# Performance work log

Measured on AMD Instinct MI355X. Metric: run time of the kernel, lower is better.

## Reference

```python
import math
import jax, jax.numpy as jnp
import numpy as np

B, T, M, S, D, H = 16, 512, 8, 32, 256, 4
HD = D // H


def setup_inputs() -> dict:
    key = jax.random.key(0)
    ks = jax.random.split(key, 16)
    w = 1.0 / math.sqrt(D)
    return {
        'q_temporal': jax.random.normal(ks[0], (B, T, M, D), jnp.float32),
        'q_static': jax.random.normal(ks[1], (B, S, D), jnp.float32),
        'k_temporal': jax.random.normal(ks[2], (B, T, M, D), jnp.float32),
        'v_temporal': jax.random.normal(ks[3], (B, T, M, D), jnp.float32),
        'k_static': jax.random.normal(ks[4], (B, S, D), jnp.float32),
        'v_static': jax.random.normal(ks[5], (B, S, D), jnp.float32),
        'q_w': jax.random.normal(ks[6], (D, D), jnp.float32) * w,
        'q_b': jax.random.normal(ks[7], (D,), jnp.float32) * w,
        'k_w': jax.random.normal(ks[8], (D, D), jnp.float32) * w,
        'k_b': jax.random.normal(ks[9], (D,), jnp.float32) * w,
        'v_w': jax.random.normal(ks[10], (D, D), jnp.float32) * w,
        'v_b': jax.random.normal(ks[11], (D,), jnp.float32) * w,
        'o_w': jax.random.normal(ks[12], (D, D), jnp.float32) * w,
        'o_b': jax.random.normal(ks[13], (D,), jnp.float32) * w,
        'mask_temporal': jax.random.randint(ks[14], (B, T, M), 0, 2).astype(jnp.int32),
        'mask_fcst': jax.random.randint(ks[15], (B, T, M), 0, 2).astype(jnp.int32),
        'mask_static': jnp.ones((B, S), jnp.int32),
    }


def _lin(x, w, b):
    # torch.nn.Linear: y = x @ W^T + b
    return x @ w.T + b


def reference(q_temporal, q_static, k_temporal, v_temporal, k_static, v_static,
              q_w, q_b, k_w, k_b, v_w, v_b, o_w, o_b,
              mask_temporal, mask_fcst, mask_static):
    scale = 1.0 / math.sqrt(HD)

    def heads5(x):  # [B,T,M,D] -> [B,H,T,M,HD]
        return x.reshape(B, T, M, H, HD).transpose(0, 3, 1, 2, 4)

    def heads3(x):  # [B,S,D] -> [B,H,S,HD]
        return x.reshape(B, -1, H, HD).transpose(0, 2, 1, 3)

    Qt = heads5(_lin(q_temporal, q_w, q_b))
    Kt = heads5(_lin(k_temporal, k_w, k_b))
    Vt = heads5(_lin(v_temporal, v_w, v_b))
    Qs = heads3(_lin(q_static, q_w, q_b))
    Ks = heads3(_lin(k_static, k_w, k_b))
    Vs = heads3(_lin(v_static, v_w, v_b))

    # additive masks: 0 where valid (==1), -inf where padded
    mt = jnp.where(mask_temporal == 1, 0.0, -jnp.inf).astype(Qt.dtype)  # [B,T,M]
    ms = jnp.where(mask_static == 1, 0.0, -jnp.inf).astype(Qt.dtype)    # [B,S]

    # ---- temporal query branch ----
    # temp_temp: per-timestep modality-vs-modality attention, column key mask
    Qt_Kt = jnp.einsum('bhtmd,bhtnd->bhtmn', Qt, Kt) * scale + mt[:, None, :, None, :]
    # temp_static: temporal queries vs static keys
    Qt_Ks = jnp.einsum('bhtmd,bhsd->bhtms', Qt, Ks) * scale + ms[:, None, None, None, :]
    tw = jax.nn.softmax(jnp.concatenate([Qt_Kt, Qt_Ks], axis=-1), axis=-1)  # [B,H,T,M,M+S]
    QKV_t = (jnp.einsum('bhtmn,bhtnd->bhtmd', tw[..., :M], Vt)
             + jnp.einsum('bhtms,bhsd->bhtmd', tw[..., M:], Vs))
    out_t = _lin(QKV_t.transpose(0, 2, 3, 1, 4).reshape(B, T, M, D), o_w, o_b)

    # ---- static query branch ----
    Ktf = Kt.reshape(B, H, T * M, HD)  # flatten (T,M) key axis
    Vtf = Vt.reshape(B, H, T * M, HD)
    Qs_Kt = jnp.einsum('bhqd,bhkd->bhqk', Qs, Ktf) * scale + mt.reshape(B, 1, 1, T * M)
    Qs_Ks = jnp.einsum('bhqd,bhsd->bhqs', Qs, Ks) * scale + ms[:, None, None, :]
    sw = jax.nn.softmax(jnp.concatenate([Qs_Kt, Qs_Ks], axis=-1), axis=-1)  # [B,H,S,T*M+S]
    QKV_s = (jnp.einsum('bhqk,bhkd->bhqd', sw[..., :T * M], Vtf)
             + jnp.einsum('bhqs,bhsd->bhqd', sw[..., T * M:], Vs))
    out_s = _lin(QKV_s.transpose(0, 2, 1, 3).reshape(B, S, D), o_w, o_b)

    return (out_t, out_s, tw, sw)
```

## Files before the change

kernel.cpp:

```cpp
#include <hip/hip_runtime.h>

#define B_   16
#define T_   512
#define M_   8
#define S_   32
#define D_   256
#define H_   4
#define HD_  64
#define TM_  4096
#define NKT  40
#define NKS  4128

typedef unsigned short u16;
typedef __attribute__((ext_vector_type(8))) short bf16x8;
typedef __attribute__((ext_vector_type(4))) float f32x4;

__device__ __forceinline__ u16 f2b(float f) {
    union { float f; unsigned u; } v; v.f = f;
    unsigned r = v.u + 0x7FFF + ((v.u >> 16) & 1);
    return (u16)(r >> 16);
}
__device__ __forceinline__ float blo(unsigned u) {
    union { unsigned i; float f; } v; v.i = u << 16; return v.f;
}
__device__ __forceinline__ float bhi(unsigned u) {
    union { unsigned i; float f; } v; v.i = u & 0xFFFF0000u; return v.f;
}
__device__ __forceinline__ float b2f(u16 u) {
    union { unsigned i; float f; } v; v.i = ((unsigned)u) << 16; return v.f;
}
__device__ __forceinline__ unsigned pack2(float lo, float hi) {
    return (unsigned)f2b(lo) | ((unsigned)f2b(hi) << 16);
}
__device__ __forceinline__ uint4 cvt8(float4 a, float4 b) {
    uint4 r;
    r.x = pack2(a.x, a.y); r.y = pack2(a.z, a.w);
    r.z = pack2(b.x, b.y); r.w = pack2(b.z, b.w);
    return r;
}

#define GLL16(g, l) __builtin_amdgcn_global_load_lds( \
    (const __attribute__((address_space(1))) void*)(g), \
    (__attribute__((address_space(3))) void*)(l), 16, 0, 0)

__global__ __launch_bounds__(256) void k_cvt_w(const float* __restrict__ W0,
                                               const float* __restrict__ W1,
                                               const float* __restrict__ W2,
                                               u16* __restrict__ dst)
{
    const int sel = blockIdx.y;
    const float* W = sel == 0 ? W0 : sel == 1 ? W1 : W2;
    u16* d = dst + sel * 65536;
    const int i0 = (blockIdx.x * 256 + threadIdx.x) * 8;
    const float4 a = *(const float4*)(W + i0);
    const float4 b = *(const float4*)(W + i0 + 4);
    *(uint4*)(d + i0) = cvt8(a, b);
}

template<int XBF, int OUTF32>
__device__ __forceinline__ void gemm_body(const void* __restrict__ Xv,
                                          const u16* __restrict__ Wb,
                                          const float* __restrict__ bias,
                                          void* __restrict__ Yv,
                                          int bx, u16* smem)
{
    u16* sA = smem;
    u16* sB = smem + 4096;
    const int tid = threadIdx.x;
    const size_t r0 = (size_t)bx * 64;
    const int wave = tid >> 6, lane = tid & 63;
    const int rbase = lane & 15, kseg = (lane >> 4) * 8;
    const int arow = tid >> 2, aseg = tid & 3;

    f32x4 acc[4][4];
#pragma unroll
    for (int i = 0; i < 4; ++i)
#pragma unroll
        for (int j = 0; j < 4; ++j) acc[i][j] = (f32x4){0, 0, 0, 0};

#define LOAD_A_F32(k0, dst) {                                                    \
        const float* gA = (const float*)Xv + (r0 + arow) * 256 + (k0) + aseg * 8; \
        dst = cvt8(*(const float4*)gA, *(const float4*)(gA + 4));                \
    }
#define STAGE_B_GLL(k0, bi)                                                      \
    _Pragma("unroll")                                                            \
    for (int i = 0; i < 4; ++i) {                                                \
        const int s = i * 256 + tid;                                             \
        GLL16(Wb + (size_t)(s >> 2) * 256 + (k0) + (s & 3) * 8,                  \
              sB + (bi) * 8192 + (i * 256 + wave * 64) * 8);                     \
    }
#define STAGE_A_GLL(k0, bi)                                                      \
    GLL16((const u16*)Xv + (r0 + arow) * 256 + (k0) + aseg * 8,                  \
          sA + (bi) * 2048 + wave * 512);

    {
        if (XBF) { STAGE_A_GLL(0, 0) }
        else { uint4 aC; LOAD_A_F32(0, aC) *(uint4*)(sA + tid * 8) = aC; }
        STAGE_B_GLL(0, 0)
    }

    for (int k = 0; k < 8; ++k) {
        const int cur = k & 1;
        __syncthreads();
        uint4 aN;
        if (k < 7) {
            const int k0n = (k + 1) * 32;
            if (XBF) { STAGE_A_GLL(k0n, cur ^ 1) }
            else     { LOAD_A_F32(k0n, aN) }
            STAGE_B_GLL(k0n, cur ^ 1)
        }
        const u16* A  = sA + cur * 2048;
        const u16* Bb = sB + cur * 8192;
        bf16x8 a[4], b[4];
#pragma unroll
        for (int f = 0; f < 4; ++f)
            a[f] = *(const bf16x8*)(A + (f * 16 + rbase) * 32 + kseg);
#pragma unroll
        for (int f = 0; f < 4; ++f)
            b[f] = *(const bf16x8*)(Bb + (wave * 64 + f * 16 + rbase) * 32 + kseg);
#pragma unroll
        for (int rf = 0; rf < 4; ++rf)
#pragma unroll
            for (int cf = 0; cf < 4; ++cf)
                acc[rf][cf] = __builtin_amdgcn_mfma_f32_16x16x32_bf16(
                    a[rf], b[cf], acc[rf][cf], 0, 0, 0);
        if (k < 7 && !XBF)
            *(uint4*)(sA + (cur ^ 1) * 2048 + tid * 8) = aN;
    }
#undef LOAD_A_F32
#undef STAGE_B_GLL
#undef STAGE_A_GLL

    const int orow = (lane >> 4) * 4, ocol = lane & 15;
    if (OUTF32) {
#pragma unroll
        for (int cf = 0; cf < 4; ++cf) {
            const int col = wave * 64 + cf * 16 + ocol;
            const float bv = bias[col];
#pragma unroll
            for (int rf = 0; rf < 4; ++rf)
#pragma unroll
                for (int r = 0; r < 4; ++r)
                    ((float*)Yv)[(r0 + rf * 16 + orow + r) * 256 + col] =
                        acc[rf][cf][r] + bv;
        }
    } else {
        __syncthreads();
#pragma unroll
        for (int cf = 0; cf < 4; ++cf) {
            const int col = wave * 64 + cf * 16 + ocol;
            const float bv = bias[col];
#pragma unroll
            for (int rf = 0; rf < 4; ++rf)
#pragma unroll
                for (int r = 0; r < 4; ++r)
                    smem[(rf * 16 + orow + r) * 256 + col] = f2b(acc[rf][cf][r] + bv);
        }
        __syncthreads();
#pragma unroll
        for (int i = 0; i < 8; ++i) {
            const int s = i * 256 + tid;
            *(uint4*)((u16*)Yv + r0 * 256 + (size_t)s * 8) = *(const uint4*)(smem + s * 8);
        }
    }
}

template<int XBF, int OUTF32>
__global__ __launch_bounds__(256) void k_gemm_m(const void* __restrict__ Xv,
                                                const u16* __restrict__ Wb,
                                                const float* __restrict__ bias,
                                                void* __restrict__ Yv)
{
    __shared__ __align__(16) u16 smem[20480];
    gemm_body<XBF, OUTF32>(Xv, Wb, bias, Yv, blockIdx.x, smem);
}

__global__ __launch_bounds__(256) void k_gemm_qkv(
    const float* __restrict__ X0, const float* __restrict__ X1, const float* __restrict__ X2,
    const u16* __restrict__ Wb,
    const float* __restrict__ b0, const float* __restrict__ b1, const float* __restrict__ b2,
    u16* __restrict__ Y0, u16* __restrict__ Y1, u16* __restrict__ Y2)
{
    __shared__ __align__(16) u16 smem[20480];
    const int sel = blockIdx.y;
    const float* X = sel == 0 ? X0 : sel == 1 ? X1 : X2;
    const float* bb = sel == 0 ? b0 : sel == 1 ? b1 : b2;
    u16* Y = sel == 0 ? Y0 : sel == 1 ? Y1 : Y2;
    gemm_body<0, 0>(X, Wb + sel * 65536, bb, Y, blockIdx.x, smem);
}

__global__ __launch_bounds__(256) void k_attn_t(
    const u16* __restrict__ Qt, const u16* __restrict__ Kt, const u16* __restrict__ Vt,
    const u16* __restrict__ Ks, const u16* __restrict__ Vs,
    const int* __restrict__ maskT, const int* __restrict__ maskS,
    float* __restrict__ tw, u16* __restrict__ qkvt)
{
    const int tp = blockIdx.x, b = blockIdx.y;
    const int t0 = tp * 2;
    __shared__ __align__(16) u16 sQ [4 * 2 * 16 * 32];
    __shared__ __align__(16) u16 sKT[4 * 2 * 16 * 32];
    __shared__ __align__(16) u16 sKS[4 * 2 * 32 * 32];
    __shared__ __align__(16) u16 sVT[4 * 64 * 72];
    __shared__ __align__(16) u16 sP [4 * 16 * 72];
    __shared__ int smT[2][8];
    __shared__ int smS[32];
    const int tid = threadIdx.x;

#pragma unroll
    for (int i = 0; i < 2; ++i) {
        const int fl = tid + i * 256;
        const int r = fl >> 5, c32 = fl & 31;
        const int h = c32 >> 3, ks = (c32 >> 2) & 1, seg = c32 & 3;
        const size_t src = (((size_t)b * T_ + t0 + (r >> 3)) * 8 + (r & 7)) * 256 + c32 * 8;
        const int dst = h * 1024 + ks * 512 + r * 32 + seg * 8;
        *(uint4*)(sQ  + dst) = *(const uint4*)(Qt + src);
        *(uint4*)(sKT + dst) = *(const uint4*)(Kt + src);
    }
#pragma unroll
    for (int i = 0; i < 4; ++i) {
        const int fl = tid + i * 256;
        const int r = fl >> 5, c32 = fl & 31;
        const int h = c32 >> 3, ks = (c32 >> 2) & 1, seg = c32 & 3;
        *(uint4*)(sKS + h * 2048 + ks * 1024 + r * 32 + seg * 8) =
            *(const uint4*)(Ks + ((size_t)b * S_ + r) * 256 + c32 * 8);
    }
    {
        const int key = tid & 63, dg = tid >> 6;
        const u16* vrow = nullptr;
        if (key < 16)      vrow = Vt + (((size_t)b * T_ + t0 + (key >> 3)) * 8 + (key & 7)) * 256;
        else if (key < 48) vrow = Vs + ((size_t)b * S_ + (key - 16)) * 256;
#pragma unroll
        for (int i = 0; i < 8; ++i) {
            const int dseg = dg * 8 + i;
            uint4 v = {0, 0, 0, 0};
            if (vrow) v = *(const uint4*)(vrow + dseg * 8);
            const int h = dseg >> 3, dl0 = (dseg & 7) * 8;
            const u16* pv = (const u16*)&v;
#pragma unroll
            for (int j = 0; j < 8; ++j)
                sVT[h * 4608 + (dl0 + j) * 72 + key] = pv[j];
        }
    }
    if (tid < 16) smT[tid >> 3][tid & 7] =
        maskT[((size_t)b * T_ + t0 + (tid >> 3)) * 8 + (tid & 7)];
    if (tid < 32) smS[tid] = maskS[b * S_ + tid];
    __syncthreads();

    const int h = tid >> 6, lane = tid & 63;
    const int c = lane & 15, g = lane >> 4, th = g >> 1;

    f32x4 at = {0,0,0,0}, as0 = {0,0,0,0}, as1 = {0,0,0,0};
#pragma unroll
    for (int ks = 0; ks < 2; ++ks) {
        bf16x8 aq = *(const bf16x8*)(sQ  + h * 1024 + ks * 512 + c * 32 + g * 8);
        bf16x8 bt = *(const bf16x8*)(sKT + h * 1024 + ks * 512 + c * 32 + g * 8);
        bf16x8 b0 = *(const bf16x8*)(sKS + h * 2048 + ks * 1024 + c * 32 + g * 8);
        bf16x8 b1 = *(const bf16x8*)(sKS + h * 2048 + ks * 1024 + 512 + c * 32 + g * 8);
        at  = __builtin_amdgcn_mfma_f32_16x16x32_bf16(aq, bt, at, 0, 0, 0);
        as0 = __builtin_amdgcn_mfma_f32_16x16x32_bf16(aq, b0, as0, 0, 0, 0);
        as1 = __builtin_amdgcn_mfma_f32_16x16x32_bf16(aq, b1, as1, 0, 0, 0);
    }

    const int vt = ((c >> 3) == th) ? smT[th][c & 7] : 0;
    const int v0 = smS[c], v1 = smS[16 + c];
    float st[4], s0[4], s1[4], mx[4];
#pragma unroll
    for (int r = 0; r < 4; ++r) {
        st[r] = vt ? at[r]  * 0.125f : -1e30f;
        s0[r] = v0 ? as0[r] * 0.125f : -1e30f;
        s1[r] = v1 ? as1[r] * 0.125f : -1e30f;
        mx[r] = fmaxf(fmaxf(st[r], s0[r]), s1[r]);
    }
#pragma unroll
    for (int o = 1; o < 16; o <<= 1)
#pragma unroll
        for (int r = 0; r < 4; ++r) mx[r] = fmaxf(mx[r], __shfl_xor(mx[r], o));
    float pt[4], p0[4], p1[4], sum[4];
#pragma unroll
    for (int r = 0; r < 4; ++r) {
        pt[r] = __expf(st[r] - mx[r]);
        p0[r] = __expf(s0[r] - mx[r]);
        p1[r] = __expf(s1[r] - mx[r]);
        sum[r] = pt[r] + p0[r] + p1[r];
    }
#pragma unroll
    for (int o = 1; o < 16; o <<= 1)
#pragma unroll
        for (int r = 0; r < 4; ++r) sum[r] += __shfl_xor(sum[r], o);
#pragma unroll
    for (int r = 0; r < 4; ++r) {
        const float inv = 1.0f / sum[r];
        pt[r] *= inv; p0[r] *= inv; p1[r] *= inv;
    }

#pragma unroll
    for (int r = 0; r < 4; ++r) {
        const int row = g * 4 + r;
        const int tt = t0 + (row >> 3), m = row & 7;
        float* twp = tw + ((((size_t)b * H_ + h) * T_ + tt) * 8 + m) * NKT;
        if ((c >> 3) == th) twp[c & 7] = pt[r];
        twp[8 + c]  = p0[r];
        twp[24 + c] = p1[r];
        u16* sp = sP + h * 1152 + row * 72;
        sp[c]      = f2b(pt[r]);
        sp[16 + c] = f2b(p0[r]);
        sp[32 + c] = f2b(p1[r]);
        sp[48 + c] = 0;
    }

    f32x4 o4[4] = {{0,0,0,0}, {0,0,0,0}, {0,0,0,0}, {0,0,0,0}};
#pragma unroll
    for (int ks = 0; ks < 2; ++ks) {
        bf16x8 pa = *(const bf16x8*)(sP + h * 1152 + c * 72 + ks * 32 + g * 8);
#pragma unroll
        for (int dt = 0; dt < 4; ++dt) {
            bf16x8 pb = *(const bf16x8*)(sVT + h * 4608 + (dt * 16 + c) * 72 + ks * 32 + g * 8);
            o4[dt] = __builtin_amdgcn_mfma_f32_16x16x32_bf16(pa, pb, o4[dt], 0, 0, 0);
        }
    }
#pragma unroll
    for (int dt = 0; dt < 4; ++dt)
#pragma unroll
        for (int r = 0; r < 4; ++r) {
            const int row = g * 4 + r;
            const int tt = t0 + (row >> 3), m = row & 7;
            qkvt[(((size_t)b * T_ + tt) * 8 + m) * 256 + h * 64 + dt * 16 + c] = f2b(o4[dt][r]);
        }
}

__global__ __launch_bounds__(256) void k_attn_s_scores(
    const u16* __restrict__ Qs, const u16* __restrict__ Kt, const u16* __restrict__ Ks,
    const int* __restrict__ maskT, const int* __restrict__ maskS,
    float* __restrict__ raw)
{
    const int ch = blockIdx.x, h = blockIdx.y, b = blockIdx.z;
    const int nk = (ch < 32) ? 128 : 32;
    const int k0 = ch * 128;
    __shared__ __align__(16) u16 sQ[2 * 32 * 32];
    __shared__ __align__(16) u16 sK[2 * 128 * 32];
    __shared__ int sM[128];
    const int tid = threadIdx.x;

    {   const int q = tid >> 3, c8 = tid & 7;
        const int ks = c8 >> 2, seg = c8 & 3;
        *(uint4*)(sQ + ks * 1024 + q * 32 + seg * 8) =
            *(const uint4*)(Qs + ((size_t)b * S_ + q) * 256 + h * 64 + c8 * 8);
    }
#pragma unroll
    for (int i = 0; i < 4; ++i) {
        const int fl = tid + i * 256;
        const int key = fl >> 3, c8 = fl & 7;
        const int ks = c8 >> 2, seg = c8 & 3;
        if (key < nk) {
            const u16* src = (ch < 32)
                ? (Kt + ((size_t)b * TM_ + k0 + key) * 256 + h * 64 + c8 * 8)
                : (Ks + ((size_t)b * S_  +      key) * 256 + h * 64 + c8 * 8);
            *(uint4*)(sK + ks * 4096 + key * 32 + seg * 8) = *(const uint4*)src;
        }
    }
    if (tid < nk) sM[tid] = (ch < 32) ? maskT[(size_t)b * TM_ + k0 + tid]
                                      : maskS[b * S_ + tid];
    __syncthreads();

    const int w = tid >> 6, lane = tid & 63;
    if (w * 32 >= nk) return;
    const int c = lane & 15, g = lane >> 4;

    f32x4 acc[2][2] = {{{0,0,0,0}, {0,0,0,0}}, {{0,0,0,0}, {0,0,0,0}}};
#pragma unroll
    for (int ks = 0; ks < 2; ++ks) {
        bf16x8 a0 = *(const bf16x8*)(sQ + ks * 1024 +        c * 32 + g * 8);
        bf16x8 a1 = *(const bf16x8*)(sQ + ks * 1024 + 512 +  c * 32 + g * 8);
        bf16x8 b0 = *(const bf16x8*)(sK + ks * 4096 + (w * 32 +      c) * 32 + g * 8);
        bf16x8 b1 = *(const bf16x8*)(sK + ks * 4096 + (w * 32 + 16 + c) * 32 + g * 8);
        acc[0][0] = __builtin_amdgcn_mfma_f32_16x16x32_bf16(a0, b0, acc[0][0], 0, 0, 0);
        acc[0][1] = __builtin_amdgcn_mfma_f32_16x16x32_bf16(a0, b1, acc[0][1], 0, 0, 0);
        acc[1][0] = __builtin_amdgcn_mfma_f32_16x16x32_bf16(a1, b0, acc[1][0], 0, 0, 0);
        acc[1][1] = __builtin_amdgcn_mfma_f32_16x16x32_bf16(a1, b1, acc[1][1], 0, 0, 0);
    }
#pragma unroll
    for (int rt = 0; rt < 2; ++rt)
#pragma unroll
        for (int ct = 0; ct < 2; ++ct) {
            const int kl = w * 32 + ct * 16 + c;
            const float madd = sM[kl] ? 0.f : -1e30f;
#pragma unroll
            for (int r = 0; r < 4; ++r) {
                const int q = rt * 16 + g * 4 + r;
                raw[(((size_t)b * H_ + h) * S_ + q) * NKS + k0 + kl] =
                    acc[rt][ct][r] * 0.125f + madd;
            }
        }
}

__global__ __launch_bounds__(256) void k_attn_s_softmax(
    const float* __restrict__ raw, float* __restrict__ sw)
{
    const int q = blockIdx.x, h = blockIdx.y, b = blockIdx.z;
    __shared__ float sRow[NKS];
    __shared__ float red[8];
    const int tid = threadIdx.x;
    const size_t base = (((size_t)b * H_ + h) * S_ + q) * NKS;

    float mx = -1e30f;
    for (int i = tid; i < NKS; i += 256) {
        const float v = raw[base + i];
        sRow[i] = v;
        mx = fmaxf(mx, v);
    }
    for (int o = 32; o; o >>= 1) mx = fmaxf(mx, __shfl_xor(mx, o));
    if ((tid & 63) == 0) red[tid >> 6] = mx;
    __syncthreads();
    mx = fmaxf(fmaxf(red[0], red[1]), fmaxf(red[2], red[3]));

    float sum = 0.f;
    for (int i = tid; i < NKS; i += 256) {
        const float e = __expf(sRow[i] - mx);
        sRow[i] = e;
        sum += e;
    }
    for (int o = 32; o; o >>= 1) sum += __shfl_xor(sum, o);
    if ((tid & 63) == 0) red[4 + (tid >> 6)] = sum;
    __syncthreads();
    sum = (red[4] + red[5]) + (red[6] + red[7]);
    const float inv = 1.0f / sum;

    for (int i = tid; i < NKS; i += 256)
        sw[base + i] = sRow[i] * inv;
}

__global__ __launch_bounds__(256) void k_attn_s_pv_part(
    const float* __restrict__ w, const u16* __restrict__ Vt, const u16* __restrict__ Vs,
    float* __restrict__ part)
{
    const int ch = blockIdx.x, h = blockIdx.y, b = blockIdx.z;
    const int nk = (ch < 32) ? 128 : 32;
    const int k0 = ch * 128;
    __shared__ float sW[32][132];
    __shared__ __align__(16) u16 sV[128 * 64];
    const int tid = threadIdx.x;

#pragma unroll
    for (int i = 0; i < 4; ++i) {
        const int fl = tid + i * 256;
        const int q = fl >> 5, k4 = fl & 31;
        if (k4 * 4 < nk)
            *(float4*)&sW[q][k4 * 4] =
                *(const float4*)(w + (((size_t)b * H_ + h) * S_ + q) * NKS + k0 + k4 * 4);
    }
#pragma unroll
    for (int i = 0; i < 4; ++i) {
        const int fl = tid + i * 256;
        const int key = fl >> 3, pp = fl & 7;
        if (key < nk) {
            const u16* src = (ch < 32)
                ? (Vt + ((size_t)b * TM_ + k0 + key) * D_ + h * HD_ + pp * 8)
                : (Vs + ((size_t)b * S_  +      key) * D_ + h * HD_ + pp * 8);
            ((uint4*)sV)[fl] = *(const uint4*)src;
        }
    }
    __syncthreads();

    const int d = tid & 63, qg = tid >> 6;
    float acc[8] = {0,0,0,0,0,0,0,0};
    for (int kk = 0; kk < nk; kk += 4) {
        const float v0 = b2f(sV[(kk + 0) * 64 + d]);
        const float v1 = b2f(sV[(kk + 1) * 64 + d]);
        const float v2 = b2f(sV[(kk + 2) * 64 + d]);
        const float v3 = b2f(sV[(kk + 3) * 64 + d]);
#pragma unroll
        for (int j = 0; j < 8; ++j) {
            const float4 wv = *(const float4*)&sW[qg * 8 + j][kk];
            acc[j] += wv.x * v0 + wv.y * v1 + wv.z * v2 + wv.w * v3;
        }
    }

    float* pb = part + (((size_t)ch * B_ + b) * H_ + h) * 2048;
#pragma unroll
    for (int j = 0; j < 8; ++j)
        pb[(qg * 8 + j) * 64 + d] = acc[j];
}

__global__ __launch_bounds__(256) void k_attn_s_pv_red(
    const float* __restrict__ part, u16* __restrict__ qkvs)
{
    const int h = blockIdx.x, b = blockIdx.y;
    const int tid = threadIdx.x;
    for (int i = tid; i < 2048; i += 256) {
        float s = 0.f;
#pragma unroll
        for (int c = 0; c < 33; ++c)
            s += part[(((size_t)c * B_ + b) * H_ + h) * 2048 + i];
        const int q = i >> 6, d = i & 63;
        qkvs[((size_t)b * S_ + q) * D_ + h * HD_ + d] = f2b(s);
    }
}

extern "C" void kernel_launch(void* const* d_in, const int* in_sizes, int n_in,
                              void* d_out, int out_size, void* d_ws, size_t ws_size,
                              hipStream_t stream)
{
    const float* q_t = (const float*)d_in[0];
    const float* q_s = (const float*)d_in[1];
    const float* k_t = (const float*)d_in[2];
    const float* v_t = (const float*)d_in[3];
    const float* k_s = (const float*)d_in[4];
    const float* v_s = (const float*)d_in[5];
    const float* q_w = (const float*)d_in[6];
    const float* q_b = (const float*)d_in[7];
    const float* k_w = (const float*)d_in[8];
    const float* k_b = (const float*)d_in[9];
    const float* v_w = (const float*)d_in[10];
    const float* v_b = (const float*)d_in[11];
    const float* o_w = (const float*)d_in[12];
    const float* o_b = (const float*)d_in[13];
    const int* maskT = (const int*)d_in[14];
    const int* maskS = (const int*)d_in[16];
    float* out = (float*)d_out;

    char* ws = (char*)d_ws;
    u16*   Kt   = (u16*)(ws + 0);
    u16*   Vt   = (u16*)(ws + 33554432);
    u16*   QKVt = (u16*)(ws + 67108864);
    float* part = (float*)(ws + 67108864);
    u16*   Wqkv = (u16*)(ws + 67108864);
    u16*   Qs   = (u16*)(ws + 100663296);
    u16*   Ks   = (u16*)(ws + 100925440);
    u16*   Vs   = (u16*)(ws + 101187584);
    u16*   QKVs = (u16*)(ws + 101449728);
    u16*   Qt   = (u16*)(ws + 101711872);
    float* raw  = (float*)(ws + 101711872);
    u16*   Wo   = (u16*)(ws + 101711872);
    if (ws_size < 135528448) return;

    float* out_t = out;
    float* out_s = out + 16777216;
    float* tw    = out + 16908288;
    float* sw    = out + 27394048;

    const dim3 blk(256);
    k_cvt_w<<<dim3(32, 3), blk, 0, stream>>>(q_w, k_w, v_w, Wqkv);

    k_gemm_qkv<<<dim3(1024, 3), blk, 0, stream>>>(q_t, k_t, v_t, Wqkv,
                                                  q_b, k_b, v_b, Qt, Kt, Vt);
    k_gemm_qkv<<<dim3(8, 3),    blk, 0, stream>>>(q_s, k_s, v_s, Wqkv,
                                                  q_b, k_b, v_b, Qs, Ks, Vs);

    k_attn_t<<<dim3(256, 16), blk, 0, stream>>>(Qt, Kt, Vt, Ks, Vs, maskT, maskS, tw, QKVt);

    k_cvt_w<<<dim3(32, 1), blk, 0, stream>>>(o_w, o_w, o_w, Wo);
    k_gemm_m<1,1><<<dim3(1024), blk, 0, stream>>>(QKVt, Wo, o_b, out_t);

    k_attn_s_scores<<<dim3(33, 4, 16), blk, 0, stream>>>(Qs, Kt, Ks, maskT, maskS, raw);
    k_attn_s_softmax<<<dim3(32, 4, 16), blk, 0, stream>>>(raw, sw);
    k_cvt_w<<<dim3(32, 1), blk, 0, stream>>>(o_w, o_w, o_w, Wo);
    k_attn_s_pv_part<<<dim3(33, 4, 16), blk, 0, stream>>>(sw, Vt, Vs, part);
    k_attn_s_pv_red<<<dim3(4, 16), blk, 0, stream>>>(part, QKVs);

    k_gemm_m<1,1><<<dim3(8),    blk, 0, stream>>>(QKVs, Wo, o_b, out_s);
}
```

Measured before the change: 257.5 us.

## Double GEMM row tile to 128 and swizzle LDS layouts to avoid bank conflicts

Each GEMM block now computes 128 output rows instead of 64, halving the grid and doubling reuse of each staged weight tile. Global-to-LDS loads use an XOR swizzle on the k-segment, and the fp32 A path writes to a padded row stride of 40, both meant to cut LDS bank conflicts. The bf16 output epilogue is split into two 64-row halves with a padded stride of 264. Launch bounds now ask for 2 blocks per CU. In exchange, the 8x4 accumulator array raises register pressure and LDS per block grows, which can lower occupancy.

```diff
diff --git a/kernel.cpp b/kernel.cpp
--- a/kernel.cpp
+++ b/kernel.cpp
@@ -64,124 +64,143 @@
                                           void* __restrict__ Yv,
                                           int bx, u16* smem)
 {
+    const int tid = threadIdx.x;
+    const size_t r0 = (size_t)bx * 128;
+    const int wave = tid >> 6, lane = tid & 63;
+    const int c = lane & 15, g = lane >> 4;
+    const int swzk = g ^ ((c >> 1) & 3);
+    const int swzl = (lane & 3) ^ ((lane >> 3) & 3);
+    const int ABUF = XBF ? 4096 : 5120;
     u16* sA = smem;
-    u16* sB = smem + 4096;
-    const int tid = threadIdx.x;
-    const size_t r0 = (size_t)bx * 64;
-    const int wave = tid >> 6, lane = tid & 63;
-    const int rbase = lane & 15, kseg = (lane >> 4) * 8;
-    const int arow = tid >> 2, aseg = tid & 3;
-
-    f32x4 acc[4][4];
-#pragma unroll
-    for (int i = 0; i < 4; ++i)
+    u16* sB = smem + 2 * ABUF;
+    const int ar = tid >> 1, ah = tid & 1;
+
+    f32x4 acc[8][4];
+#pragma unroll
+    for (int i = 0; i < 8; ++i)
 #pragma unroll
         for (int j = 0; j < 4; ++j) acc[i][j] = (f32x4){0, 0, 0, 0};
 
-#define LOAD_A_F32(k0, dst) {                                                    \
-        const float* gA = (const float*)Xv + (r0 + arow) * 256 + (k0) + aseg * 8; \
-        dst = cvt8(*(const float4*)gA, *(const float4*)(gA + 4));                \
-    }
-#define STAGE_B_GLL(k0, bi)                                                      \
-    _Pragma("unroll")                                                            \
-    for (int i = 0; i < 4; ++i) {                                                \
-        const int s = i * 256 + tid;                                             \
-        GLL16(Wb + (size_t)(s >> 2) * 256 + (k0) + (s & 3) * 8,                  \
-              sB + (bi) * 8192 + (i * 256 + wave * 64) * 8);                     \
-    }
-#define STAGE_A_GLL(k0, bi)                                                      \
-    GLL16((const u16*)Xv + (r0 + arow) * 256 + (k0) + aseg * 8,                  \
-          sA + (bi) * 2048 + wave * 512);
-
+#define STAGE_B(k0, bi)                                                         \
+    _Pragma("unroll")                                                           \
+    for (int i = 0; i < 4; ++i) {                                               \
+        const int row = i * 64 + wave * 16 + (lane >> 2);                       \
+        GLL16(Wb + (size_t)row * 256 + (k0) + swzl * 8,                         \
+              sB + (bi) * 8192 + (i * 256 + wave * 64) * 8);                    \
+    }
+#define STAGE_A_GLL(k0, bi)                                                     \
+    _Pragma("unroll")                                                           \
+    for (int i = 0; i < 2; ++i) {                                               \
+        const int row = i * 64 + wave * 16 + (lane >> 2);                       \
+        GLL16((const u16*)Xv + (r0 + row) * 256 + (k0) + swzl * 8,              \
+              sA + (bi) * 4096 + (i * 256 + wave * 64) * 8);                    \
+    }
+#define LOAD_A_F32(k0, fa)                                                      \
+    {   const float* gA = (const float*)Xv + (r0 + ar) * 256 + (k0) + ah * 16;  \
+        fa[0] = *(const float4*)gA;       fa[1] = *(const float4*)(gA + 4);     \
+        fa[2] = *(const float4*)(gA + 8); fa[3] = *(const float4*)(gA + 12);    \
+    }
+#define WRITE_A(bi, fa)                                                         \
+    {   u16* d = sA + (bi) * 5120 + ar * 40 + ah * 16;                          \
+        *(uint4*)d       = cvt8(fa[0], fa[1]);                                  \
+        *(uint4*)(d + 8) = cvt8(fa[2], fa[3]);                                  \
+    }
+
+    float4 fa[4];
     {
         if (XBF) { STAGE_A_GLL(0, 0) }
-        else { uint4 aC; LOAD_A_F32(0, aC) *(uint4*)(sA + tid * 8) = aC; }
-        STAGE_B_GLL(0, 0)
+        else     { LOAD_A_F32(0, fa) WRITE_A(0, fa) }
+        STAGE_B(0, 0)
     }
 
     for (int k = 0; k < 8; ++k) {
         const int cur = k & 1;
         __syncthreads();
-        uint4 aN;
         if (k < 7) {
             const int k0n = (k + 1) * 32;
             if (XBF) { STAGE_A_GLL(k0n, cur ^ 1) }
-            else     { LOAD_A_F32(k0n, aN) }
-            STAGE_B_GLL(k0n, cur ^ 1)
-        }
-        const u16* A  = sA + cur * 2048;
-        const u16* Bb = sB + cur * 8192;
-        bf16x8 a[4], b[4];
+            else     { LOAD_A_F32(k0n, fa) }
+            STAGE_B(k0n, cur ^ 1)
+        }
+        bf16x8 a[8], b[4];
+#pragma unroll
+        for (int f = 0; f < 8; ++f)
+            a[f] = XBF
+                ? *(const bf16x8*)(sA + cur * 4096 + (f * 16 + c) * 32 + swzk * 8)
+                : *(const bf16x8*)(sA + cur * 5120 + (f * 16 + c) * 40 + g * 8);
 #pragma unroll
         for (int f = 0; f < 4; ++f)
-            a[f] = *(const bf16x8*)(A + (f * 16 + rbase) * 32 + kseg);
-#pragma unroll
-        for (int f = 0; f < 4; ++f)
-            b[f] = *(const bf16x8*)(Bb + (wave * 64 + f * 16 + rbase) * 32 + kseg);
-#pragma unroll
-        for (int rf = 0; rf < 4; ++rf)
+            b[f] = *(const bf16x8*)(sB + cur * 8192 + (wave * 64 + f * 16 + c) * 32 + swzk * 8);
+#pragma unroll
+        for (int rf = 0; rf < 8; ++rf)
 #pragma unroll
             for (int cf = 0; cf < 4; ++cf)
                 acc[rf][cf] = __builtin_amdgcn_mfma_f32_16x16x32_bf16(
                     a[rf], b[cf], acc[rf][cf], 0, 0, 0);
-        if (k < 7 && !XBF)
-            *(uint4*)(sA + (cur ^ 1) * 2048 + tid * 8) = aN;
-    }
+        if (k < 7 && !XBF) WRITE_A(cur ^ 1, fa)
+    }
+#undef STAGE_B
+#undef STAGE_A_GLL
 #undef LOAD_A_F32
-#undef STAGE_B_GLL
-#undef STAGE_A_GLL
-
-    const int orow = (lane >> 4) * 4, ocol = lane & 15;
+#undef WRITE_A
+
+    const int orow = g * 4, ocol = c;
     if (OUTF32) {
 #pragma unroll
         for (int cf = 0; cf < 4; ++cf) {
             const int col = wave * 64 + cf * 16 + ocol;
             const float bv = bias[col];
 #pragma unroll
-            for (int rf = 0; rf < 4; ++rf)
+            for (int rf = 0; rf < 8; ++rf)
 #pragma unroll
                 for (int r = 0; r < 4; ++r)
                     ((float*)Yv)[(r0 + rf * 16 + orow + r) * 256 + col] =
                         acc[rf][cf][r] + bv;
         }
     } else {
-        __syncthreads();
-#pragma unroll
-        for (int cf = 0; cf < 4; ++cf) {
-            const int col = wave * 64 + cf * 16 + ocol;
-            const float bv = bias[col];
-#pragma unroll
-            for (int rf = 0; rf < 4; ++rf)
-#pragma unroll
-                for (int r = 0; r < 4; ++r)
-                    smem[(rf * 16 + orow + r) * 256 + col] = f2b(acc[rf][cf][r] + bv);
-        }
-        __syncthreads();
-#pragma unroll
-        for (int i = 0; i < 8; ++i) {
-            const int s = i * 256 + tid;
-            *(uint4*)((u16*)Yv + r0 * 256 + (size_t)s * 8) = *(const uint4*)(smem + s * 8);
+#pragma unroll
+        for (int hh = 0; hh < 2; ++hh) {
+            __syncthreads();
+#pragma unroll
+            for (int cf = 0; cf < 4; ++cf) {
+                const int col = wave * 64 + cf * 16 + ocol;
+                const float bv = bias[col];
+#pragma unroll
+                for (int rf4 = 0; rf4 < 4; ++rf4)
+#pragma unroll
+                    for (int r = 0; r < 4; ++r)
+                        smem[(rf4 * 16 + orow + r) * 264 + col] =
+                            f2b(acc[hh * 4 + rf4][cf][r] + bv);
+            }
+            __syncthreads();
+#pragma unroll
+            for (int i = 0; i < 8; ++i) {
+                const int s = i * 256 + tid;
+                const int row = s >> 5, seg = s & 31;
+                *(uint4*)((u16*)Yv + (r0 + hh * 64 + row) * 256 + seg * 8) =
+                    *(const uint4*)(smem + row * 264 + seg * 8);
+            }
         }
     }
 }
 
 template<int XBF, int OUTF32>
-__global__ __launch_bounds__(256) void k_gemm_m(const void* __restrict__ Xv,
-                                                const u16* __restrict__ Wb,
-                                                const float* __restrict__ bias,
-                                                void* __restrict__ Yv)
-{
-    __shared__ __align__(16) u16 smem[20480];
+__global__ __launch_bounds__(256, 2) void k_gemm_m(const void* __restrict__ Xv,
+                                                   const u16* __restrict__ Wb,
+                                                   const float* __restrict__ bias,
+                                                   void* __restrict__ Yv)
+{
+    __shared__ __align__(16) u16 smem[26624];
     gemm_body<XBF, OUTF32>(Xv, Wb, bias, Yv, blockIdx.x, smem);
 }
 
-__global__ __launch_bounds__(256) void k_gemm_qkv(
+__global__ __launch_bounds__(256, 2) void k_gemm_qkv(
     const float* __restrict__ X0, const float* __restrict__ X1, const float* __restrict__ X2,
     const u16* __restrict__ Wb,
     const float* __restrict__ b0, const float* __restrict__ b1, const float* __restrict__ b2,
     u16* __restrict__ Y0, u16* __restrict__ Y1, u16* __restrict__ Y2)
 {
-    __shared__ __align__(16) u16 smem[20480];
+    __shared__ __align__(16) u16 smem[26624];
     const int sel = blockIdx.y;
     const float* X = sel == 0 ? X0 : sel == 1 ? X1 : X2;
     const float* bb = sel == 0 ? b0 : sel == 1 ? b1 : b2;
@@ -541,15 +560,15 @@
     const dim3 blk(256);
     k_cvt_w<<<dim3(32, 3), blk, 0, stream>>>(q_w, k_w, v_w, Wqkv);
 
-    k_gemm_qkv<<<dim3(1024, 3), blk, 0, stream>>>(q_t, k_t, v_t, Wqkv,
-                                                  q_b, k_b, v_b, Qt, Kt, Vt);
-    k_gemm_qkv<<<dim3(8, 3),    blk, 0, stream>>>(q_s, k_s, v_s, Wqkv,
-                                                  q_b, k_b, v_b, Qs, Ks, Vs);
+    k_gemm_qkv<<<dim3(512, 3), blk, 0, stream>>>(q_t, k_t, v_t, Wqkv,
+                                                 q_b, k_b, v_b, Qt, Kt, Vt);
+    k_gemm_qkv<<<dim3(4, 3),   blk, 0, stream>>>(q_s, k_s, v_s, Wqkv,
+                                                 q_b, k_b, v_b, Qs, Ks, Vs);
 
     k_attn_t<<<dim3(256, 16), blk, 0, stream>>>(Qt, Kt, Vt, Ks, Vs, maskT, maskS, tw, QKVt);
 
     k_cvt_w<<<dim3(32, 1), blk, 0, stream>>>(o_w, o_w, o_w, Wo);
-    k_gemm_m<1,1><<<dim3(1024), blk, 0, stream>>>(QKVt, Wo, o_b, out_t);
+    k_gemm_m<1,1><<<dim3(512), blk, 0, stream>>>(QKVt, Wo, o_b, out_t);
 
     k_attn_s_scores<<<dim3(33, 4, 16), blk, 0, stream>>>(Qs, Kt, Ks, maskT, maskS, raw);
     k_attn_s_softmax<<<dim3(32, 4, 16), blk, 0, stream>>>(raw, sw);
@@ -557,5 +576,5 @@
     k_attn_s_pv_part<<<dim3(33, 4, 16), blk, 0, stream>>>(sw, Vt, Vs, part);
     k_attn_s_pv_red<<<dim3(4, 16), blk, 0, stream>>>(part, QKVs);
 
-    k_gemm_m<1,1><<<dim3(8),    blk, 0, stream>>>(QKVs, Wo, o_b, out_s);
-}
+    k_gemm_m<1,1><<<dim3(4),   blk, 0, stream>>>(QKVs, Wo, o_b, out_s);
+}
```

Result: no change. 262.0 us (+1.8%).
